# Kernel tuning notes

Measured on AMD Instinct MI355X. Metric: run time of the kernel, lower is better.

The kernel has to match this reference:

```python
import jax, jax.numpy as jnp
import numpy as np

NUM_GROUPS = 8
EPS = 1e-5


def group_norm(x, gamma, beta):
    # x: [B, C, H, W]
    B, C, H, W = x.shape
    xg = x.reshape(B, NUM_GROUPS, C // NUM_GROUPS, H, W)
    mean = xg.mean(axis=(2, 3, 4), keepdims=True)
    var = xg.var(axis=(2, 3, 4), keepdims=True)
    xn = ((xg - mean) * jax.lax.rsqrt(var + EPS)).reshape(B, C, H, W)
    return xn * gamma[None, :, None, None] + beta[None, :, None, None]


def conv1x1(x, w, b):
    # x: [B, C, H, W], w: [Cout, Cin], b: [Cout]
    return jnp.einsum('bchw,oc->bohw', x, w) + b[None, :, None, None]


def setup_inputs() -> dict:
    key = jax.random.key(0)
    ks = jax.random.split(key, 7)
    C = 128
    x = jax.random.normal(ks[0], (4, C, 64, 64), dtype=jnp.float32)
    norm_w = jnp.ones((C,), dtype=jnp.float32)
    norm_b = jnp.zeros((C,), dtype=jnp.float32)
    s = 1.0 / np.sqrt(C)
    qkv_w = jax.random.normal(ks[1], (3 * C, C), dtype=jnp.float32) * s
    qkv_b = jax.random.normal(ks[2], (3 * C,), dtype=jnp.float32) * 0.01
    proj_w = jax.random.normal(ks[3], (C, C), dtype=jnp.float32) * s
    proj_b = jax.random.normal(ks[4], (C,), dtype=jnp.float32) * 0.01
    return {"x": x, "norm_w": norm_w, "norm_b": norm_b,
            "qkv_w": qkv_w, "qkv_b": qkv_b,
            "proj_w": proj_w, "proj_b": proj_b}


def reference(x, norm_w, norm_b, qkv_w, qkv_b, proj_w, proj_b):
    B, C, H, W = x.shape
    qkv = conv1x1(group_norm(x, norm_w, norm_b), qkv_w, qkv_b)
    q, k, v = jnp.split(qkv, 3, axis=1)           # each [B, C, H, W]
    q = q.reshape(B, C, H * W).transpose(0, 2, 1)  # [B, HW, C]
    k = k.reshape(B, C, H * W)                     # [B, C, HW]
    v = v.reshape(B, C, H * W).transpose(0, 2, 1)  # [B, HW, C]
    scale = 1.0 / np.sqrt(C).astype(np.float32)
    attn = jax.nn.softmax(jnp.einsum('bnc,bcm->bnm', q, k) * scale, axis=-1)
    out = jnp.einsum('bnm,bmc->bnc', attn, v)      # [B, HW, C]
    out = out.transpose(0, 2, 1).reshape(B, C, H, W)
    return x + conv1x1(out, proj_w, proj_b)
```

## Files before the change

### kernel.cpp

```cpp
#include <hip/hip_runtime.h>

typedef unsigned short u16;
typedef unsigned int   u32;

#define HW 4096
#define NC 128

typedef __bf16 bf16x8 __attribute__((ext_vector_type(8)));
typedef float  f32x16 __attribute__((ext_vector_type(16)));

__device__ __forceinline__ bf16x8 as_bf8(uint4 u){
    union { uint4 u; bf16x8 b; } c; c.u = u; return c.b;
}
__device__ __forceinline__ u32 pack2(float a, float b){
    return ((__float_as_uint(a) + 0x8000u) >> 16) | ((__float_as_uint(b) + 0x8000u) & 0xffff0000u);
}
__device__ __forceinline__ float bf_lo(u32 u){ return __uint_as_float(u << 16); }
__device__ __forceinline__ float bf_hi(u32 u){ return __uint_as_float(u & 0xffff0000u); }

__device__ __forceinline__ float exp2_hw(float x){ return __builtin_amdgcn_exp2f(x); }

__device__ __forceinline__ void plswap(u32 &a, u32 &b){
    asm("v_permlane32_swap_b32 %0, %1" : "+v"(a), "+v"(b));
}
__device__ __forceinline__ u32 cvtpk(float a, float b){
    u32 r; asm("v_cvt_pk_bf16_f32 %0, %1, %2" : "=v"(r) : "v"(a), "v"(b)); return r;
}

__global__ __launch_bounds__(256) void gnw_kernel(const float* __restrict__ x,
                                                  float* __restrict__ stats,
                                                  const float* __restrict__ qkv_w,
                                                  const float* __restrict__ proj_w,
                                                  uint4* __restrict__ Wf,
                                                  uint4* __restrict__ Pf){
    if (blockIdx.x < 256){
        int bg = blockIdx.x >> 3, part = blockIdx.x & 7;
        const float4* p = (const float4*)(x + (size_t)bg * 65536 + part * 8192);
        float s = 0.f, ss = 0.f;
        #pragma unroll
        for (int i = 0; i < 8; i++){
            float4 u = p[threadIdx.x + i*256];
            s  += u.x + u.y + u.z + u.w;
            ss += u.x*u.x + u.y*u.y + u.z*u.z + u.w*u.w;
        }
        #pragma unroll
        for (int off = 32; off > 0; off >>= 1){
            s  += __shfl_xor(s,  off);
            ss += __shfl_xor(ss, off);
        }
        __shared__ float rs[4], rss[4];
        int wid = threadIdx.x >> 6;
        if ((threadIdx.x & 63) == 0){ rs[wid] = s; rss[wid] = ss; }
        __syncthreads();
        if (threadIdx.x == 0){
            stats[bg*16 + part*2]     = rs[0]+rs[1]+rs[2]+rs[3];
            stats[bg*16 + part*2 + 1] = rss[0]+rss[1]+rss[2]+rss[3];
        }
    } else {
        int id = (blockIdx.x - 256)*256 + threadIdx.x;
        const float* src; uint4* dst; int fi;
        if (id < 6144){ src = qkv_w; dst = Wf; fi = id; }
        else          { src = proj_w; dst = Pf; fi = id - 6144; }
        int l = fi & 63, ks = (fi >> 6) & 7, ob = fi >> 9;
        int o = ob*32 + (l & 31);
        int c = ks*16 + ((l >> 5) << 3);
        const float* s = src + o*128 + c;
        dst[fi] = make_uint4(pack2(s[0],s[1]), pack2(s[2],s[3]), pack2(s[4],s[5]), pack2(s[6],s[7]));
    }
}

__global__ __launch_bounds__(256) void qkv_kernel(const float* __restrict__ x,
                                                  const float* __restrict__ stats,
                                                  const float* __restrict__ gamma,
                                                  const float* __restrict__ beta,
                                                  const uint4* __restrict__ Wf,
                                                  const float* __restrict__ bias,
                                                  uint4* __restrict__ Qf,
                                                  uint4* __restrict__ Kf,
                                                  uint4* __restrict__ Vf){
    __shared__ float gaL[128], beL[128], biasL[384];
    __shared__ uint4 xfL[512];
    int b = blockIdx.x >> 7, tokblk = blockIdx.x & 127;
    int t = threadIdx.x, lane = t & 63, wv = t >> 6;
    if (t < 128){
        int g = t >> 4;
        float S = 0.f, SS = 0.f;
        #pragma unroll
        for (int p = 0; p < 8; p++){
            S  += stats[(b*8 + g)*16 + p*2];
            SS += stats[(b*8 + g)*16 + p*2 + 1];
        }
        float mean = S * (1.f/65536.f);
        float rstd = rsqrtf(SS * (1.f/65536.f) - mean*mean + 1e-5f);
        float ga = gamma[t] * rstd;
        gaL[t] = ga; beL[t] = beta[t] - mean*ga;
    }
    if (t < 192){ biasL[t] = bias[t]; biasL[t+192] = bias[t+192]; }
    __syncthreads();

    #pragma unroll
    for (int rr = 0; rr < 2; rr++){
        int f = rr*256 + t;
        int ks = f >> 6, ln = f & 63;
        int h2 = ln >> 5, tl2 = ln & 31;
        int c0 = ks*16 + h2*8;
        const float* xb = x + ((size_t)b*128 + c0)*HW + tokblk*32 + tl2;
        float4 g0 = *(float4*)&gaL[c0], g1 = *(float4*)&gaL[c0+4];
        float4 e0 = *(float4*)&beL[c0], e1 = *(float4*)&beL[c0+4];
        float v[8];
        #pragma unroll
        for (int j = 0; j < 8; j++) v[j] = xb[(size_t)j*HW];
        v[0] = fmaf(v[0], g0.x, e0.x); v[1] = fmaf(v[1], g0.y, e0.y);
        v[2] = fmaf(v[2], g0.z, e0.z); v[3] = fmaf(v[3], g0.w, e0.w);
        v[4] = fmaf(v[4], g1.x, e1.x); v[5] = fmaf(v[5], g1.y, e1.y);
        v[6] = fmaf(v[6], g1.z, e1.z); v[7] = fmaf(v[7], g1.w, e1.w);
        xfL[f] = make_uint4(pack2(v[0],v[1]), pack2(v[2],v[3]), pack2(v[4],v[5]), pack2(v[6],v[7]));
    }
    __syncthreads();

    int h = lane >> 5, tl = lane & 31;
    uint4 xf[8];
    #pragma unroll
    for (int ks = 0; ks < 8; ks++) xf[ks] = xfL[ks*64 + lane];

    bool up = (lane >= 32);
    #pragma unroll
    for (int i = 0; i < 3; i++){
        int ob = wv*3 + i;
        uint4 wf[8];
        #pragma unroll
        for (int ks = 0; ks < 8; ks++) wf[ks] = Wf[(ob*8 + ks)*64 + lane];
        f32x16 D;
        #pragma unroll
        for (int r = 0; r < 16; r++) D[r] = 0.f;
        if (ob < 8){
            #pragma unroll
            for (int ks = 0; ks < 8; ks++)
                D = __builtin_amdgcn_mfma_f32_32x32x16_bf16(as_bf8(wf[ks]), as_bf8(xf[ks]), D, 0,0,0);
            #pragma unroll
            for (int r = 0; r < 16; r++)
                D[r] += biasL[ob*32 + (r&3) + 8*(r>>2) + 4*h];
            u32 pk[8], xch[8];
            #pragma unroll
            for (int j = 0; j < 8; j++) pk[j] = pack2(D[2*j], D[2*j+1]);
            #pragma unroll
            for (int j = 0; j < 8; j++) xch[j] = __shfl_xor(pk[j], 32);
            uint4 F0 = up ? make_uint4(xch[2],xch[3],pk[2],pk[3]) : make_uint4(pk[0],pk[1],xch[0],xch[1]);
            uint4 F1 = up ? make_uint4(xch[6],xch[7],pk[6],pk[7]) : make_uint4(pk[4],pk[5],xch[4],xch[5]);
            uint4* dst = (ob < 4) ? Qf : Kf;
            int obl = ob & 3;
            size_t base = (((size_t)b*128 + tokblk)*8 + obl*2)*64 + lane;
            dst[base] = F0; dst[base + 64] = F1;
        } else {
            #pragma unroll
            for (int ks = 0; ks < 8; ks++)
                D = __builtin_amdgcn_mfma_f32_32x32x16_bf16(as_bf8(xf[ks]), as_bf8(wf[ks]), D, 0,0,0);
            int nb = ob - 8;
            float vb = biasL[256 + nb*32 + tl];
            #pragma unroll
            for (int r = 0; r < 16; r++) D[r] += vb;
            u32 pk[8], xch[8];
            #pragma unroll
            for (int j = 0; j < 8; j++) pk[j] = pack2(D[2*j], D[2*j+1]);
            #pragma unroll
            for (int j = 0; j < 8; j++) xch[j] = __shfl_xor(pk[j], 32);
            uint4 F0 = up ? make_uint4(xch[2],xch[3],pk[2],pk[3]) : make_uint4(pk[0],pk[1],xch[0],xch[1]);
            uint4 F1 = up ? make_uint4(xch[6],xch[7],pk[6],pk[7]) : make_uint4(pk[4],pk[5],xch[4],xch[5]);
            int it = tokblk >> 1, t2 = tokblk & 1;
            size_t base = ((((size_t)b*64 + it)*4 + nb)*4 + t2*2)*64 + lane;
            Vf[base] = F0; Vf[base + 64] = F1;
        }
    }
}

__global__ __launch_bounds__(256, 2) void attn_kernel(const uint4* __restrict__ Qf,
                                                      const uint4* __restrict__ Kf,
                                                      const uint4* __restrict__ Vf,
                                                      uint4* __restrict__ Opart,
                                                      float* __restrict__ lsum){
    __shared__ float fsm[8192];
    __shared__ float lred[64];
    int pair = blockIdx.x & 7, qx = blockIdx.x >> 3;
    int b = pair >> 1, ksp = pair & 1;
    int t = threadIdx.x, lane = t & 63, wv = t >> 6;
    int qh = wv >> 1, kh = wv & 1;
    const float SC2 = 0.12751744361402804f;
    const float B2  = -11.541560327111707f;

    uint4 qf[8];
    const uint4* qptr = Qf + (((size_t)b*128 + qx*2 + qh)*8)*64 + lane;
    #pragma unroll
    for (int ks = 0; ks < 8; ks++) qf[ks] = qptr[ks*64];

    f32x16 O[4];
    #pragma unroll
    for (int nb = 0; nb < 4; nb++)
        #pragma unroll
        for (int r = 0; r < 16; r++) O[nb][r] = 0.f;
    float l_i = 0.f;

    const uint4* kgw = Kf + (((size_t)b*128 + ksp*64)*8)*64 + (kh<<9) + lane;
    const uint4* vgw = Vf + (((size_t)b*64  + ksp*32)*16)*64 + (kh<<7) + lane;

    uint4 kf[8], vf[8];
    #pragma unroll
    for (int ks = 0; ks < 8; ks++) kf[ks] = kgw[ks*64];
    #pragma unroll
    for (int nb = 0; nb < 4; nb++){
        vf[nb*2]   = vgw[nb*256];
        vf[nb*2+1] = vgw[nb*256 + 64];
    }

    for (int it = 0; it < 32; it++){
        f32x16 Sa, Sb;
        #pragma unroll
        for (int r = 0; r < 16; r++){ Sa[r] = 0.f; Sb[r] = 0.f; }
        #pragma unroll
        for (int ks = 0; ks < 4; ks++)
            Sa = __builtin_amdgcn_mfma_f32_32x32x16_bf16(as_bf8(kf[ks]), as_bf8(qf[ks]), Sa, 0,0,0);
        #pragma unroll
        for (int ks = 4; ks < 8; ks++)
            Sb = __builtin_amdgcn_mfma_f32_32x32x16_bf16(as_bf8(kf[ks]), as_bf8(qf[ks]), Sb, 0,0,0);
        #pragma unroll
        for (int r = 0; r < 16; r++) Sa[r] += Sb[r];

        if (it < 31){
            const uint4* kn = kgw + (it+1)*1024;
            #pragma unroll
            for (int ks = 0; ks < 8; ks++) kf[ks] = kn[ks*64];
        }

        float psum = 0.f;
        u32 pk[8];
        #pragma unroll
        for (int q = 0; q < 4; q++){
            float e0 = exp2_hw(__fmaf_rn(Sa[q*4+0], SC2, B2));
            float e1 = exp2_hw(__fmaf_rn(Sa[q*4+1], SC2, B2));
            float e2 = exp2_hw(__fmaf_rn(Sa[q*4+2], SC2, B2));
            float e3 = exp2_hw(__fmaf_rn(Sa[q*4+3], SC2, B2));
            psum += (e0+e1)+(e2+e3);
            pk[2*q] = cvtpk(e0,e1); pk[2*q+1] = cvtpk(e2,e3);
        }
        {
            u32 ua = __float_as_uint(psum), ub = ua;
            plswap(ua, ub);
            l_i += __uint_as_float(ua) + __uint_as_float(ub);
        }

        plswap(pk[0], pk[2]); plswap(pk[1], pk[3]);
        plswap(pk[4], pk[6]); plswap(pk[5], pk[7]);
        uint4 fr0 = make_uint4(pk[0], pk[1], pk[2], pk[3]);
        uint4 fr1 = make_uint4(pk[4], pk[5], pk[6], pk[7]);

        #pragma unroll
        for (int nb = 0; nb < 4; nb++){
            O[nb] = __builtin_amdgcn_mfma_f32_32x32x16_bf16(as_bf8(vf[nb*2]),   as_bf8(fr0), O[nb], 0,0,0);
            O[nb] = __builtin_amdgcn_mfma_f32_32x32x16_bf16(as_bf8(vf[nb*2+1]), as_bf8(fr1), O[nb], 0,0,0);
        }

        if (it < 31){
            const uint4* vn = vgw + (it+1)*1024;
            #pragma unroll
            for (int nb = 0; nb < 4; nb++){
                vf[nb*2]   = vn[nb*256];
                vf[nb*2+1] = vn[nb*256 + 64];
            }
        }
    }

    if (kh == 1){
        #pragma unroll
        for (int nb = 0; nb < 4; nb++)
            #pragma unroll
            for (int r = 0; r < 16; r++)
                fsm[((qh*4+nb)*16 + r)*64 + lane] = O[nb][r];
        if (lane < 32) lred[qh*32 + lane] = l_i;
    }
    __syncthreads();
    if (kh == 0){
        float lt = l_i + lred[qh*32 + (lane & 31)];
        if (lane < 32) lsum[((size_t)(ksp*4 + b))*HW + (qx*2+qh)*32 + lane] = lt;
        bool up = (lane >= 32);
        uint4* oc = Opart + (size_t)ksp*262144 + (((size_t)b*128 + qx*2 + qh)*8)*64 + lane;
        #pragma unroll
        for (int nb = 0; nb < 4; nb++){
            #pragma unroll
            for (int r = 0; r < 16; r++) O[nb][r] += fsm[((qh*4+nb)*16 + r)*64 + lane];
            u32 pk[8], xch[8];
            #pragma unroll
            for (int j = 0; j < 8; j++) pk[j] = pack2(O[nb][2*j], O[nb][2*j+1]);
            #pragma unroll
            for (int j = 0; j < 8; j++) xch[j] = __shfl_xor(pk[j], 32);
            uint4 F0 = up ? make_uint4(xch[2],xch[3],pk[2],pk[3]) : make_uint4(pk[0],pk[1],xch[0],xch[1]);
            uint4 F1 = up ? make_uint4(xch[6],xch[7],pk[6],pk[7]) : make_uint4(pk[4],pk[5],xch[4],xch[5]);
            oc[(nb*2)*64]     = F0;
            oc[(nb*2 + 1)*64] = F1;
        }
    }
}

__global__ __launch_bounds__(256) void proj_kernel(const uint4* __restrict__ Op,
                                                   const float* __restrict__ lsum,
                                                   const uint4* __restrict__ Pf,
                                                   const float* __restrict__ bias,
                                                   const float* __restrict__ x,
                                                   float* __restrict__ out){
    __shared__ uint4 ofL[1024];
    __shared__ float biasL[128];
    int t = threadIdx.x, lane = t & 63, ob = t >> 6;
    int b = blockIdx.x >> 7, tokblk = blockIdx.x & 127;
    int h = lane >> 5, tl = lane & 31;

    {
        size_t base0 = ((size_t)b*128 + tokblk)*512;
        #pragma unroll
        for (int i = 0; i < 2; i++) ofL[i*256 + t]       = Op[base0 + i*256 + t];
        #pragma unroll
        for (int i = 0; i < 2; i++) ofL[512 + i*256 + t] = Op[262144 + base0 + i*256 + t];
    }
    if (t < 128) biasL[t] = bias[t];

    int rowg = b*HW + tokblk*32 + tl;
    float inv = 1.f / (lsum[rowg] + lsum[16384 + rowg]);

    uint4 pf[8];
    #pragma unroll
    for (int ks = 0; ks < 8; ks++) pf[ks] = Pf[(ob*8 + ks)*64 + lane];

    __syncthreads();

    f32x16 D;
    #pragma unroll
    for (int r = 0; r < 16; r++) D[r] = 0.f;
    #pragma unroll
    for (int ks = 0; ks < 8; ks++)
        D = __builtin_amdgcn_mfma_f32_32x32x16_bf16(as_bf8(pf[ks]), as_bf8(ofL[ks*64 + lane]), D, 0,0,0);
    #pragma unroll
    for (int ks = 0; ks < 8; ks++)
        D = __builtin_amdgcn_mfma_f32_32x32x16_bf16(as_bf8(pf[ks]), as_bf8(ofL[512 + ks*64 + lane]), D, 0,0,0);

    #pragma unroll
    for (int r = 0; r < 16; r++){
        int o = ob*32 + (r&3) + 8*(r>>2) + 4*h;
        size_t gi = ((size_t)b*128 + o)*HW + tokblk*32 + tl;
        out[gi] = x[gi] + biasL[o] + D[r]*inv;
    }
}

extern "C" void kernel_launch(void* const* d_in, const int* in_sizes, int n_in,
                              void* d_out, int out_size, void* d_ws, size_t ws_size,
                              hipStream_t stream){
    const float* x      = (const float*)d_in[0];
    const float* norm_w = (const float*)d_in[1];
    const float* norm_b = (const float*)d_in[2];
    const float* qkv_w  = (const float*)d_in[3];
    const float* qkv_b  = (const float*)d_in[4];
    const float* proj_w = (const float*)d_in[5];
    const float* proj_b = (const float*)d_in[6];
    float* out = (float*)d_out;

    char* w = (char*)d_ws;
    float* stats = (float*)w;
    uint4* Qf   = (uint4*)(w + 2048);
    uint4* Kf   = (uint4*)(w + 4196352);
    uint4* Vf   = (uint4*)(w + 8390656);
    float* lsum = (float*)(w + 12584960);
    uint4* Wf   = (uint4*)(w + 12716032);
    uint4* Pf   = (uint4*)(w + 12814336);
    uint4* Op2  = (uint4*)(w + 12847104);

    gnw_kernel<<<288, 256, 0, stream>>>(x, stats, qkv_w, proj_w, Wf, Pf);
    qkv_kernel<<<512, 256, 0, stream>>>(x, stats, norm_w, norm_b, Wf, qkv_b, Qf, Kf, Vf);
    attn_kernel<<<512, 256, 0, stream>>>(Qf, Kf, Vf, Op2, lsum);
    proj_kernel<<<512, 256, 0, stream>>>(Op2, lsum, Pf, proj_b, x, out);
}
```

Measured before the change: 127.7 us.

## Fuse four kernels into one cooperative persistent kernel with grid syncs

Replaces the four separate launches (stats/weight-prep, QKV projection, attention, output projection) with a single cooperative kernel of 512 blocks that separates the phases with fenced grid-wide barriers. This removes three kernel launch gaps and the tail/ramp-up between dependent kernels. In exchange, all blocks must be co-resident (launch bounds of 2 blocks per CU), grid syncs add barrier latency, and the shared smem allocation plus register pressure of the fused body may lower occupancy in the attention phase. It falls back to the original four launches if the cooperative launch fails.

```diff
diff --git a/kernel.cpp b/kernel.cpp
--- a/kernel.cpp
+++ b/kernel.cpp
@@ -1,4 +1,7 @@
 #include <hip/hip_runtime.h>
+#include <hip/hip_cooperative_groups.h>
+
+namespace cg = cooperative_groups;
 
 typedef unsigned short u16;
 typedef unsigned int   u32;
@@ -15,9 +18,6 @@
 __device__ __forceinline__ u32 pack2(float a, float b){
     return ((__float_as_uint(a) + 0x8000u) >> 16) | ((__float_as_uint(b) + 0x8000u) & 0xffff0000u);
 }
-__device__ __forceinline__ float bf_lo(u32 u){ return __uint_as_float(u << 16); }
-__device__ __forceinline__ float bf_hi(u32 u){ return __uint_as_float(u & 0xffff0000u); }
-
 __device__ __forceinline__ float exp2_hw(float x){ return __builtin_amdgcn_exp2f(x); }
 
 __device__ __forceinline__ void plswap(u32 &a, u32 &b){
@@ -25,6 +25,331 @@
 }
 __device__ __forceinline__ u32 cvtpk(float a, float b){
     u32 r; asm("v_cvt_pk_bf16_f32 %0, %1, %2" : "=v"(r) : "v"(a), "v"(b)); return r;
+}
+
+__device__ __forceinline__ void gsync_fenced(cg::grid_group& g){
+    __syncthreads();
+    if (threadIdx.x == 0) __threadfence();
+    g.sync();
+    if (threadIdx.x == 0) __threadfence();
+    __syncthreads();
+}
+
+__global__ __launch_bounds__(256, 2) void mega_kernel(const float* __restrict__ x,
+                                                      float* __restrict__ stats,
+                                                      const float* __restrict__ qkv_w,
+                                                      const float* __restrict__ proj_w,
+                                                      uint4* __restrict__ Wf,
+                                                      uint4* __restrict__ Pf,
+                                                      const float* __restrict__ gamma,
+                                                      const float* __restrict__ beta,
+                                                      const float* __restrict__ qkv_b,
+                                                      uint4* __restrict__ Qf,
+                                                      uint4* __restrict__ Kf,
+                                                      uint4* __restrict__ Vf,
+                                                      uint4* __restrict__ Op2,
+                                                      float* __restrict__ lsum,
+                                                      const float* __restrict__ proj_b,
+                                                      float* __restrict__ out){
+    cg::grid_group grid = cg::this_grid();
+    __shared__ __align__(16) char smraw[33280];
+    int t = threadIdx.x, lane = t & 63, wv = t >> 6;
+
+    if (blockIdx.x < 256){
+        float* rs  = (float*)smraw;
+        float* rss = (float*)smraw + 4;
+        int bg = blockIdx.x >> 3, part = blockIdx.x & 7;
+        const float4* p = (const float4*)(x + (size_t)bg * 65536 + part * 8192);
+        float s = 0.f, ss = 0.f;
+        #pragma unroll
+        for (int i = 0; i < 8; i++){
+            float4 u = p[t + i*256];
+            s  += u.x + u.y + u.z + u.w;
+            ss += u.x*u.x + u.y*u.y + u.z*u.z + u.w*u.w;
+        }
+        #pragma unroll
+        for (int off = 32; off > 0; off >>= 1){
+            s  += __shfl_xor(s,  off);
+            ss += __shfl_xor(ss, off);
+        }
+        if ((t & 63) == 0){ rs[wv] = s; rss[wv] = ss; }
+        __syncthreads();
+        if (t == 0){
+            stats[bg*16 + part*2]     = rs[0]+rs[1]+rs[2]+rs[3];
+            stats[bg*16 + part*2 + 1] = rss[0]+rss[1]+rss[2]+rss[3];
+        }
+    } else if (blockIdx.x < 288){
+        int id = (blockIdx.x - 256)*256 + t;
+        const float* src; uint4* dst; int fi;
+        if (id < 6144){ src = qkv_w; dst = Wf; fi = id; }
+        else          { src = proj_w; dst = Pf; fi = id - 6144; }
+        int l = fi & 63, ks = (fi >> 6) & 7, ob = fi >> 9;
+        int o = ob*32 + (l & 31);
+        int c = ks*16 + ((l >> 5) << 3);
+        const float* s = src + o*128 + c;
+        dst[fi] = make_uint4(pack2(s[0],s[1]), pack2(s[2],s[3]), pack2(s[4],s[5]), pack2(s[6],s[7]));
+    }
+    gsync_fenced(grid);
+
+    {
+        float* gaL   = (float*)smraw;
+        float* beL   = (float*)smraw + 128;
+        float* biasL = (float*)smraw + 256;
+        uint4* xfL   = (uint4*)(smraw + 2560);
+        int b = blockIdx.x >> 7, tokblk = blockIdx.x & 127;
+        if (t < 128){
+            int g = t >> 4;
+            float S = 0.f, SS = 0.f;
+            #pragma unroll
+            for (int p = 0; p < 8; p++){
+                S  += stats[(b*8 + g)*16 + p*2];
+                SS += stats[(b*8 + g)*16 + p*2 + 1];
+            }
+            float mean = S * (1.f/65536.f);
+            float rstd = rsqrtf(SS * (1.f/65536.f) - mean*mean + 1e-5f);
+            float ga = gamma[t] * rstd;
+            gaL[t] = ga; beL[t] = beta[t] - mean*ga;
+        }
+        if (t < 192){ biasL[t] = qkv_b[t]; biasL[t+192] = qkv_b[t+192]; }
+        __syncthreads();
+
+        #pragma unroll
+        for (int rr = 0; rr < 2; rr++){
+            int f = rr*256 + t;
+            int ks = f >> 6, ln = f & 63;
+            int h2 = ln >> 5, tl2 = ln & 31;
+            int c0 = ks*16 + h2*8;
+            const float* xb = x + ((size_t)b*128 + c0)*HW + tokblk*32 + tl2;
+            float4 g0 = *(float4*)&gaL[c0], g1 = *(float4*)&gaL[c0+4];
+            float4 e0 = *(float4*)&beL[c0], e1 = *(float4*)&beL[c0+4];
+            float v[8];
+            #pragma unroll
+            for (int j = 0; j < 8; j++) v[j] = xb[(size_t)j*HW];
+            v[0] = fmaf(v[0], g0.x, e0.x); v[1] = fmaf(v[1], g0.y, e0.y);
+            v[2] = fmaf(v[2], g0.z, e0.z); v[3] = fmaf(v[3], g0.w, e0.w);
+            v[4] = fmaf(v[4], g1.x, e1.x); v[5] = fmaf(v[5], g1.y, e1.y);
+            v[6] = fmaf(v[6], g1.z, e1.z); v[7] = fmaf(v[7], g1.w, e1.w);
+            xfL[f] = make_uint4(pack2(v[0],v[1]), pack2(v[2],v[3]), pack2(v[4],v[5]), pack2(v[6],v[7]));
+        }
+        __syncthreads();
+
+        int h = lane >> 5, tl = lane & 31;
+        uint4 xf[8];
+        #pragma unroll
+        for (int ks = 0; ks < 8; ks++) xf[ks] = xfL[ks*64 + lane];
+
+        bool up = (lane >= 32);
+        #pragma unroll
+        for (int i = 0; i < 3; i++){
+            int ob = wv*3 + i;
+            uint4 wf[8];
+            #pragma unroll
+            for (int ks = 0; ks < 8; ks++) wf[ks] = Wf[(ob*8 + ks)*64 + lane];
+            f32x16 D;
+            #pragma unroll
+            for (int r = 0; r < 16; r++) D[r] = 0.f;
+            if (ob < 8){
+                #pragma unroll
+                for (int ks = 0; ks < 8; ks++)
+                    D = __builtin_amdgcn_mfma_f32_32x32x16_bf16(as_bf8(wf[ks]), as_bf8(xf[ks]), D, 0,0,0);
+                #pragma unroll
+                for (int r = 0; r < 16; r++)
+                    D[r] += biasL[ob*32 + (r&3) + 8*(r>>2) + 4*h];
+                u32 pk[8], xch[8];
+                #pragma unroll
+                for (int j = 0; j < 8; j++) pk[j] = pack2(D[2*j], D[2*j+1]);
+                #pragma unroll
+                for (int j = 0; j < 8; j++) xch[j] = __shfl_xor(pk[j], 32);
+                uint4 F0 = up ? make_uint4(xch[2],xch[3],pk[2],pk[3]) : make_uint4(pk[0],pk[1],xch[0],xch[1]);
+                uint4 F1 = up ? make_uint4(xch[6],xch[7],pk[6],pk[7]) : make_uint4(pk[4],pk[5],xch[4],xch[5]);
+                uint4* dst = (ob < 4) ? Qf : Kf;
+                int obl = ob & 3;
+                size_t base = (((size_t)b*128 + tokblk)*8 + obl*2)*64 + lane;
+                dst[base] = F0; dst[base + 64] = F1;
+            } else {
+                #pragma unroll
+                for (int ks = 0; ks < 8; ks++)
+                    D = __builtin_amdgcn_mfma_f32_32x32x16_bf16(as_bf8(xf[ks]), as_bf8(wf[ks]), D, 0,0,0);
+                int nb = ob - 8;
+                float vb = biasL[256 + nb*32 + tl];
+                #pragma unroll
+                for (int r = 0; r < 16; r++) D[r] += vb;
+                u32 pk[8], xch[8];
+                #pragma unroll
+                for (int j = 0; j < 8; j++) pk[j] = pack2(D[2*j], D[2*j+1]);
+                #pragma unroll
+                for (int j = 0; j < 8; j++) xch[j] = __shfl_xor(pk[j], 32);
+                uint4 F0 = up ? make_uint4(xch[2],xch[3],pk[2],pk[3]) : make_uint4(pk[0],pk[1],xch[0],xch[1]);
+                uint4 F1 = up ? make_uint4(xch[6],xch[7],pk[6],pk[7]) : make_uint4(pk[4],pk[5],xch[4],xch[5]);
+                int it = tokblk >> 1, t2 = tokblk & 1;
+                size_t base = ((((size_t)b*64 + it)*4 + nb)*4 + t2*2)*64 + lane;
+                Vf[base] = F0; Vf[base + 64] = F1;
+            }
+        }
+    }
+    gsync_fenced(grid);
+
+    {
+        float* fsm  = (float*)smraw;
+        float* lred = (float*)(smraw + 32768);
+        int pair = blockIdx.x & 7, qx = blockIdx.x >> 3;
+        int b = pair >> 1, ksp = pair & 1;
+        int qh = wv >> 1, kh = wv & 1;
+        const float SC2 = 0.12751744361402804f;
+        const float B2  = -11.541560327111707f;
+
+        uint4 qf[8];
+        const uint4* qptr = Qf + (((size_t)b*128 + qx*2 + qh)*8)*64 + lane;
+        #pragma unroll
+        for (int ks = 0; ks < 8; ks++) qf[ks] = qptr[ks*64];
+
+        f32x16 O[4];
+        #pragma unroll
+        for (int nb = 0; nb < 4; nb++)
+            #pragma unroll
+            for (int r = 0; r < 16; r++) O[nb][r] = 0.f;
+        float l_i = 0.f;
+
+        const uint4* kgw = Kf + (((size_t)b*128 + ksp*64)*8)*64 + (kh<<9) + lane;
+        const uint4* vgw = Vf + (((size_t)b*64  + ksp*32)*16)*64 + (kh<<7) + lane;
+
+        uint4 kf[8], vf[8];
+        #pragma unroll
+        for (int ks = 0; ks < 8; ks++) kf[ks] = kgw[ks*64];
+        #pragma unroll
+        for (int nb = 0; nb < 4; nb++){
+            vf[nb*2]   = vgw[nb*256];
+            vf[nb*2+1] = vgw[nb*256 + 64];
+        }
+
+        for (int it = 0; it < 32; it++){
+            f32x16 Sa, Sb;
+            #pragma unroll
+            for (int r = 0; r < 16; r++){ Sa[r] = 0.f; Sb[r] = 0.f; }
+            #pragma unroll
+            for (int ks = 0; ks < 4; ks++)
+                Sa = __builtin_amdgcn_mfma_f32_32x32x16_bf16(as_bf8(kf[ks]), as_bf8(qf[ks]), Sa, 0,0,0);
+            #pragma unroll
+            for (int ks = 4; ks < 8; ks++)
+                Sb = __builtin_amdgcn_mfma_f32_32x32x16_bf16(as_bf8(kf[ks]), as_bf8(qf[ks]), Sb, 0,0,0);
+            #pragma unroll
+            for (int r = 0; r < 16; r++) Sa[r] += Sb[r];
+
+            if (it < 31){
+                const uint4* kn = kgw + (it+1)*1024;
+                #pragma unroll
+                for (int ks = 0; ks < 8; ks++) kf[ks] = kn[ks*64];
+            }
+
+            float psum = 0.f;
+            u32 pk[8];
+            #pragma unroll
+            for (int q = 0; q < 4; q++){
+                float e0 = exp2_hw(__fmaf_rn(Sa[q*4+0], SC2, B2));
+                float e1 = exp2_hw(__fmaf_rn(Sa[q*4+1], SC2, B2));
+                float e2 = exp2_hw(__fmaf_rn(Sa[q*4+2], SC2, B2));
+                float e3 = exp2_hw(__fmaf_rn(Sa[q*4+3], SC2, B2));
+                psum += (e0+e1)+(e2+e3);
+                pk[2*q] = cvtpk(e0,e1); pk[2*q+1] = cvtpk(e2,e3);
+            }
+            {
+                u32 ua = __float_as_uint(psum), ub = ua;
+                plswap(ua, ub);
+                l_i += __uint_as_float(ua) + __uint_as_float(ub);
+            }
+
+            plswap(pk[0], pk[2]); plswap(pk[1], pk[3]);
+            plswap(pk[4], pk[6]); plswap(pk[5], pk[7]);
+            uint4 fr0 = make_uint4(pk[0], pk[1], pk[2], pk[3]);
+            uint4 fr1 = make_uint4(pk[4], pk[5], pk[6], pk[7]);
+
+            #pragma unroll
+            for (int nb = 0; nb < 4; nb++){
+                O[nb] = __builtin_amdgcn_mfma_f32_32x32x16_bf16(as_bf8(vf[nb*2]),   as_bf8(fr0), O[nb], 0,0,0);
+                O[nb] = __builtin_amdgcn_mfma_f32_32x32x16_bf16(as_bf8(vf[nb*2+1]), as_bf8(fr1), O[nb], 0,0,0);
+            }
+
+            if (it < 31){
+                const uint4* vn = vgw + (it+1)*1024;
+                #pragma unroll
+                for (int nb = 0; nb < 4; nb++){
+                    vf[nb*2]   = vn[nb*256];
+                    vf[nb*2+1] = vn[nb*256 + 64];
+                }
+            }
+        }
+
+        if (kh == 1){
+            #pragma unroll
+            for (int nb = 0; nb < 4; nb++)
+                #pragma unroll
+                for (int r = 0; r < 16; r++)
+                    fsm[((qh*4+nb)*16 + r)*64 + lane] = O[nb][r];
+            if (lane < 32) lred[qh*32 + lane] = l_i;
+        }
+        __syncthreads();
+        if (kh == 0){
+            float lt = l_i + lred[qh*32 + (lane & 31)];
+            if (lane < 32) lsum[((size_t)(ksp*4 + b))*HW + (qx*2+qh)*32 + lane] = lt;
+            bool up = (lane >= 32);
+            uint4* oc = Op2 + (size_t)ksp*262144 + (((size_t)b*128 + qx*2 + qh)*8)*64 + lane;
+            #pragma unroll
+            for (int nb = 0; nb < 4; nb++){
+                #pragma unroll
+                for (int r = 0; r < 16; r++) O[nb][r] += fsm[((qh*4+nb)*16 + r)*64 + lane];
+                u32 pk[8], xch[8];
+                #pragma unroll
+                for (int j = 0; j < 8; j++) pk[j] = pack2(O[nb][2*j], O[nb][2*j+1]);
+                #pragma unroll
+                for (int j = 0; j < 8; j++) xch[j] = __shfl_xor(pk[j], 32);
+                uint4 F0 = up ? make_uint4(xch[2],xch[3],pk[2],pk[3]) : make_uint4(pk[0],pk[1],xch[0],xch[1]);
+                uint4 F1 = up ? make_uint4(xch[6],xch[7],pk[6],pk[7]) : make_uint4(pk[4],pk[5],xch[4],xch[5]);
+                oc[(nb*2)*64]     = F0;
+                oc[(nb*2 + 1)*64] = F1;
+            }
+        }
+    }
+    gsync_fenced(grid);
+
+    {
+        uint4* ofL   = (uint4*)smraw;
+        float* biasP = (float*)(smraw + 16384);
+        int b = blockIdx.x >> 7, tokblk = blockIdx.x & 127;
+        int ob = wv, h = lane >> 5, tl = lane & 31;
+
+        size_t base0 = ((size_t)b*128 + tokblk)*512;
+        #pragma unroll
+        for (int i = 0; i < 2; i++) ofL[i*256 + t]       = Op2[base0 + i*256 + t];
+        #pragma unroll
+        for (int i = 0; i < 2; i++) ofL[512 + i*256 + t] = Op2[262144 + base0 + i*256 + t];
+        if (t < 128) biasP[t] = proj_b[t];
+
+        int rowg = b*HW + tokblk*32 + tl;
+        float inv = 1.f / (lsum[rowg] + lsum[16384 + rowg]);
+
+        uint4 pf[8];
+        #pragma unroll
+        for (int ks = 0; ks < 8; ks++) pf[ks] = Pf[(ob*8 + ks)*64 + lane];
+
+        __syncthreads();
+
+        f32x16 D;
+        #pragma unroll
+        for (int r = 0; r < 16; r++) D[r] = 0.f;
+        #pragma unroll
+        for (int ks = 0; ks < 8; ks++)
+            D = __builtin_amdgcn_mfma_f32_32x32x16_bf16(as_bf8(pf[ks]), as_bf8(ofL[ks*64 + lane]), D, 0,0,0);
+        #pragma unroll
+        for (int ks = 0; ks < 8; ks++)
+            D = __builtin_amdgcn_mfma_f32_32x32x16_bf16(as_bf8(pf[ks]), as_bf8(ofL[512 + ks*64 + lane]), D, 0,0,0);
+
+        #pragma unroll
+        for (int r = 0; r < 16; r++){
+            int o = ob*32 + (r&3) + 8*(r>>2) + 4*h;
+            size_t gi = ((size_t)b*128 + o)*HW + tokblk*32 + tl;
+            out[gi] = x[gi] + biasP[o] + D[r]*inv;
+        }
+    }
 }
 
 __global__ __launch_bounds__(256) void gnw_kernel(const float* __restrict__ x,
@@ -369,8 +694,18 @@
     uint4* Pf   = (uint4*)(w + 12814336);
     uint4* Op2  = (uint4*)(w + 12847104);
 
-    gnw_kernel<<<288, 256, 0, stream>>>(x, stats, qkv_w, proj_w, Wf, Pf);
-    qkv_kernel<<<512, 256, 0, stream>>>(x, stats, norm_w, norm_b, Wf, qkv_b, Qf, Kf, Vf);
-    attn_kernel<<<512, 256, 0, stream>>>(Qf, Kf, Vf, Op2, lsum);
-    proj_kernel<<<512, 256, 0, stream>>>(Op2, lsum, Pf, proj_b, x, out);
-}
+    void* args[] = {
+        (void*)&x, (void*)&stats, (void*)&qkv_w, (void*)&proj_w,
+        (void*)&Wf, (void*)&Pf, (void*)&norm_w, (void*)&norm_b, (void*)&qkv_b,
+        (void*)&Qf, (void*)&Kf, (void*)&Vf, (void*)&Op2, (void*)&lsum,
+        (void*)&proj_b, (void*)&out
+    };
+    hipError_t err = hipLaunchCooperativeKernel((void*)mega_kernel, dim3(512), dim3(256),
+                                                args, 0, stream);
+    if (err != hipSuccess){
+        gnw_kernel<<<288, 256, 0, stream>>>(x, stats, qkv_w, proj_w, Wf, Pf);
+        qkv_kernel<<<512, 256, 0, stream>>>(x, stats, norm_w, norm_b, Wf, qkv_b, Qf, Kf, Vf);
+        attn_kernel<<<512, 256, 0, stream>>>(Qf, Kf, Vf, Op2, lsum);
+        proj_kernel<<<512, 256, 0, stream>>>(Op2, lsum, Pf, proj_b, x, out);
+    }
+}
```

Measured after the change: 386.7 us. +202.7%, slower.

## Fuse attention and output projection into one kernel with 4-way key split per block

Applied to the files above, without the earlier changes.

Merges the attention and projection kernels. Each 512-thread block now covers all keys for one 64-query tile, with four waves per query half splitting the key range, and reduces their partial outputs and row sums through shared memory. The projection then runs in-block from the shared-memory tile. This removes the global round trip for partial outputs and row sums plus one kernel launch. The cost is fewer blocks (256 instead of 512), one-block-per-CU occupancy, and three serialized reduction steps with barriers.

```diff
diff --git a/kernel.cpp b/kernel.cpp
--- a/kernel.cpp
+++ b/kernel.cpp
@@ -15,9 +15,6 @@
 __device__ __forceinline__ u32 pack2(float a, float b){
     return ((__float_as_uint(a) + 0x8000u) >> 16) | ((__float_as_uint(b) + 0x8000u) & 0xffff0000u);
 }
-__device__ __forceinline__ float bf_lo(u32 u){ return __uint_as_float(u << 16); }
-__device__ __forceinline__ float bf_hi(u32 u){ return __uint_as_float(u & 0xffff0000u); }
-
 __device__ __forceinline__ float exp2_hw(float x){ return __builtin_amdgcn_exp2f(x); }
 
 __device__ __forceinline__ void plswap(u32 &a, u32 &b){
@@ -173,20 +170,27 @@
     }
 }
 
-__global__ __launch_bounds__(256, 2) void attn_kernel(const uint4* __restrict__ Qf,
-                                                      const uint4* __restrict__ Kf,
-                                                      const uint4* __restrict__ Vf,
-                                                      uint4* __restrict__ Opart,
-                                                      float* __restrict__ lsum){
+__global__ __launch_bounds__(512, 1) void attnproj_kernel(const uint4* __restrict__ Qf,
+                                                          const uint4* __restrict__ Kf,
+                                                          const uint4* __restrict__ Vf,
+                                                          const uint4* __restrict__ Pf,
+                                                          const float* __restrict__ pbias,
+                                                          const float* __restrict__ x,
+                                                          float* __restrict__ out){
     __shared__ float fsm[8192];
-    __shared__ float lred[64];
-    int pair = blockIdx.x & 7, qx = blockIdx.x >> 3;
-    int b = pair >> 1, ksp = pair & 1;
+    __shared__ uint4 ofL[1024];
+    __shared__ float lredL[64];
+    __shared__ float invL[64];
+    __shared__ float biasP[128];
+
     int t = threadIdx.x, lane = t & 63, wv = t >> 6;
-    int qh = wv >> 1, kh = wv & 1;
+    int qh = wv & 1, kh = wv >> 1;
+    int b = blockIdx.x & 3, qx = blockIdx.x >> 2;
     const float SC2 = 0.12751744361402804f;
     const float B2  = -11.541560327111707f;
 
+    if (t < 128) biasP[t] = pbias[t];
+
     uint4 qf[8];
     const uint4* qptr = Qf + (((size_t)b*128 + qx*2 + qh)*8)*64 + lane;
     #pragma unroll
@@ -199,8 +203,8 @@
         for (int r = 0; r < 16; r++) O[nb][r] = 0.f;
     float l_i = 0.f;
 
-    const uint4* kgw = Kf + (((size_t)b*128 + ksp*64)*8)*64 + (kh<<9) + lane;
-    const uint4* vgw = Vf + (((size_t)b*64  + ksp*32)*16)*64 + (kh<<7) + lane;
+    const uint4* kgw = Kf + (size_t)b*65536 + kh*512 + lane;
+    const uint4* vgw = Vf + (size_t)b*65536 + (kh>>1)*1024 + (kh&1)*128 + lane;
 
     uint4 kf[8], vf[8];
     #pragma unroll
@@ -225,7 +229,7 @@
         for (int r = 0; r < 16; r++) Sa[r] += Sb[r];
 
         if (it < 31){
-            const uint4* kn = kgw + (it+1)*1024;
+            const uint4* kn = kgw + (size_t)(it+1)*2048;
             #pragma unroll
             for (int ks = 0; ks < 8; ks++) kf[ks] = kn[ks*64];
         }
@@ -259,7 +263,7 @@
         }
 
         if (it < 31){
-            const uint4* vn = vgw + (it+1)*1024;
+            const uint4* vn = vgw + (size_t)(it+1)*2048;
             #pragma unroll
             for (int nb = 0; nb < 4; nb++){
                 vf[nb*2]   = vn[nb*256];
@@ -268,20 +272,36 @@
         }
     }
 
-    if (kh == 1){
+    if (kh == 3){
         #pragma unroll
         for (int nb = 0; nb < 4; nb++)
             #pragma unroll
             for (int r = 0; r < 16; r++)
                 fsm[((qh*4+nb)*16 + r)*64 + lane] = O[nb][r];
-        if (lane < 32) lred[qh*32 + lane] = l_i;
+        if (lane < 32) lredL[qh*32 + lane] = l_i;
+    }
+    __syncthreads();
+    if (kh == 2){
+        #pragma unroll
+        for (int nb = 0; nb < 4; nb++)
+            #pragma unroll
+            for (int r = 0; r < 16; r++)
+                fsm[((qh*4+nb)*16 + r)*64 + lane] += O[nb][r];
+        if (lane < 32) lredL[qh*32 + lane] += l_i;
+    }
+    __syncthreads();
+    if (kh == 1){
+        #pragma unroll
+        for (int nb = 0; nb < 4; nb++)
+            #pragma unroll
+            for (int r = 0; r < 16; r++)
+                fsm[((qh*4+nb)*16 + r)*64 + lane] += O[nb][r];
+        if (lane < 32) lredL[qh*32 + lane] += l_i;
     }
     __syncthreads();
     if (kh == 0){
-        float lt = l_i + lred[qh*32 + (lane & 31)];
-        if (lane < 32) lsum[((size_t)(ksp*4 + b))*HW + (qx*2+qh)*32 + lane] = lt;
+        float lt = l_i + lredL[qh*32 + (lane & 31)];
         bool up = (lane >= 32);
-        uint4* oc = Opart + (size_t)ksp*262144 + (((size_t)b*128 + qx*2 + qh)*8)*64 + lane;
         #pragma unroll
         for (int nb = 0; nb < 4; nb++){
             #pragma unroll
@@ -293,57 +313,33 @@
             for (int j = 0; j < 8; j++) xch[j] = __shfl_xor(pk[j], 32);
             uint4 F0 = up ? make_uint4(xch[2],xch[3],pk[2],pk[3]) : make_uint4(pk[0],pk[1],xch[0],xch[1]);
             uint4 F1 = up ? make_uint4(xch[6],xch[7],pk[6],pk[7]) : make_uint4(pk[4],pk[5],xch[4],xch[5]);
-            oc[(nb*2)*64]     = F0;
-            oc[(nb*2 + 1)*64] = F1;
-        }
-    }
-}
-
-__global__ __launch_bounds__(256) void proj_kernel(const uint4* __restrict__ Op,
-                                                   const float* __restrict__ lsum,
-                                                   const uint4* __restrict__ Pf,
-                                                   const float* __restrict__ bias,
-                                                   const float* __restrict__ x,
-                                                   float* __restrict__ out){
-    __shared__ uint4 ofL[1024];
-    __shared__ float biasL[128];
-    int t = threadIdx.x, lane = t & 63, ob = t >> 6;
-    int b = blockIdx.x >> 7, tokblk = blockIdx.x & 127;
-    int h = lane >> 5, tl = lane & 31;
+            ofL[qh*512 + nb*128 + lane]      = F0;
+            ofL[qh*512 + nb*128 + 64 + lane] = F1;
+        }
+        if (lane < 32) invL[qh*32 + lane] = 1.f / lt;
+    }
+    __syncthreads();
 
     {
-        size_t base0 = ((size_t)b*128 + tokblk)*512;
-        #pragma unroll
-        for (int i = 0; i < 2; i++) ofL[i*256 + t]       = Op[base0 + i*256 + t];
-        #pragma unroll
-        for (int i = 0; i < 2; i++) ofL[512 + i*256 + t] = Op[262144 + base0 + i*256 + t];
-    }
-    if (t < 128) biasL[t] = bias[t];
-
-    int rowg = b*HW + tokblk*32 + tl;
-    float inv = 1.f / (lsum[rowg] + lsum[16384 + rowg]);
-
-    uint4 pf[8];
-    #pragma unroll
-    for (int ks = 0; ks < 8; ks++) pf[ks] = Pf[(ob*8 + ks)*64 + lane];
-
-    __syncthreads();
-
-    f32x16 D;
-    #pragma unroll
-    for (int r = 0; r < 16; r++) D[r] = 0.f;
-    #pragma unroll
-    for (int ks = 0; ks < 8; ks++)
-        D = __builtin_amdgcn_mfma_f32_32x32x16_bf16(as_bf8(pf[ks]), as_bf8(ofL[ks*64 + lane]), D, 0,0,0);
-    #pragma unroll
-    for (int ks = 0; ks < 8; ks++)
-        D = __builtin_amdgcn_mfma_f32_32x32x16_bf16(as_bf8(pf[ks]), as_bf8(ofL[512 + ks*64 + lane]), D, 0,0,0);
-
-    #pragma unroll
-    for (int r = 0; r < 16; r++){
-        int o = ob*32 + (r&3) + 8*(r>>2) + 4*h;
-        size_t gi = ((size_t)b*128 + o)*HW + tokblk*32 + tl;
-        out[gi] = x[gi] + biasL[o] + D[r]*inv;
+        int tb = wv >> 2, ob = wv & 3;
+        int h = lane >> 5, tl = lane & 31;
+        uint4 pf[8];
+        #pragma unroll
+        for (int ks = 0; ks < 8; ks++) pf[ks] = Pf[(ob*8 + ks)*64 + lane];
+        f32x16 D;
+        #pragma unroll
+        for (int r = 0; r < 16; r++) D[r] = 0.f;
+        #pragma unroll
+        for (int ks = 0; ks < 8; ks++)
+            D = __builtin_amdgcn_mfma_f32_32x32x16_bf16(as_bf8(pf[ks]), as_bf8(ofL[tb*512 + ks*64 + lane]), D, 0,0,0);
+        float inv = invL[tb*32 + tl];
+        int tokblk = qx*2 + tb;
+        #pragma unroll
+        for (int r = 0; r < 16; r++){
+            int o = ob*32 + (r&3) + 8*(r>>2) + 4*h;
+            size_t gi = ((size_t)b*128 + o)*HW + tokblk*32 + tl;
+            out[gi] = x[gi] + biasP[o] + D[r]*inv;
+        }
     }
 }
 
@@ -364,13 +360,10 @@
     uint4* Qf   = (uint4*)(w + 2048);
     uint4* Kf   = (uint4*)(w + 4196352);
     uint4* Vf   = (uint4*)(w + 8390656);
-    float* lsum = (float*)(w + 12584960);
     uint4* Wf   = (uint4*)(w + 12716032);
     uint4* Pf   = (uint4*)(w + 12814336);
-    uint4* Op2  = (uint4*)(w + 12847104);
 
     gnw_kernel<<<288, 256, 0, stream>>>(x, stats, qkv_w, proj_w, Wf, Pf);
     qkv_kernel<<<512, 256, 0, stream>>>(x, stats, norm_w, norm_b, Wf, qkv_b, Qf, Kf, Vf);
-    attn_kernel<<<512, 256, 0, stream>>>(Qf, Kf, Vf, Op2, lsum);
-    proj_kernel<<<512, 256, 0, stream>>>(Op2, lsum, Pf, proj_b, x, out);
-}
+    attnproj_kernel<<<256, 512, 0, stream>>>(Qf, Kf, Vf, Pf, proj_b, x, out);
+}
```

Measured after the change: 129.1 us. Within noise of the previous version (+1.1%).
